# Optimization experiments

Measured on AMD Instinct MI355X. Metric: run time of the kernel, lower is better.

## Reference

```python
import jax, jax.numpy as jnp
import numpy as np

N = 10000
E = 160000
IN_DIM = 128
OUT_DIM = 32
HEADS = 32
H1 = OUT_DIM * 2   # 64 per-head channels in layer 1
H2 = OUT_DIM       # 32 per-head channels in layer 2
NEG_SLOPE = 0.2
EPS = 1e-16  # PyG softmax denominator epsilon


def gat_layer(x, src, dst, W, a_src, a_dst, b, n_nodes, heads, ch):
    # x: [N, F_in], W: [F_in, heads*ch], a_src/a_dst: [heads, ch], b: [ch]
    xp = (x @ W).reshape(n_nodes, heads, ch)                 # [N,H,C]
    alpha_s = jnp.einsum('nhc,hc->nh', xp, a_src)            # [N,H]
    alpha_d = jnp.einsum('nhc,hc->nh', xp, a_dst)            # [N,H]
    e = jax.nn.leaky_relu(alpha_s[src] + alpha_d[dst], NEG_SLOPE)  # [E,H]
    # segment softmax over edges grouped by destination node
    m = jax.ops.segment_max(e, dst, num_segments=n_nodes)    # [N,H]
    e = jnp.exp(e - m[dst])                                  # [E,H]
    s = jax.ops.segment_sum(e, dst, num_segments=n_nodes)    # [N,H]
    alpha = e / (s[dst] + EPS)                               # [E,H]
    msg = alpha[:, :, None] * xp[src]                        # [E,H,C]
    out = jax.ops.segment_sum(msg, dst, num_segments=n_nodes)  # [N,H,C]
    return out.mean(axis=1) + b                              # concat=False: head mean, [N,C]


def setup_inputs() -> dict:
    key = jax.random.key(0)
    ks = jax.random.split(key, 9)
    x = jax.random.normal(ks[0], (N, IN_DIM), dtype=jnp.float32)
    edge_index = jax.random.randint(ks[1], (2, E), 0, N, dtype=jnp.int64)
    W1 = jax.random.normal(ks[2], (IN_DIM, HEADS * H1), dtype=jnp.float32) * 0.1
    a_src1 = jax.random.normal(ks[3], (HEADS, H1), dtype=jnp.float32) * 0.1
    a_dst1 = jax.random.normal(ks[4], (HEADS, H1), dtype=jnp.float32) * 0.1
    b1 = jnp.zeros((H1,), dtype=jnp.float32)
    W2 = jax.random.normal(ks[5], (H1, HEADS * H2), dtype=jnp.float32) * 0.1
    a_src2 = jax.random.normal(ks[6], (HEADS, H2), dtype=jnp.float32) * 0.1
    a_dst2 = jax.random.normal(ks[7], (HEADS, H2), dtype=jnp.float32) * 0.1
    b2 = jnp.zeros((H2,), dtype=jnp.float32)
    return {"x": x, "edge_index": edge_index,
            "W1": W1, "a_src1": a_src1, "a_dst1": a_dst1, "b1": b1,
            "W2": W2, "a_src2": a_src2, "a_dst2": a_dst2, "b2": b2}


def reference(x, edge_index, W1, a_src1, a_dst1, b1, W2, a_src2, a_dst2, b2):
    # flow='source_to_target': messages go edge_index[0] -> edge_index[1]
    src = edge_index[0]
    dst = edge_index[1]
    z1 = jax.nn.elu(gat_layer(x, src, dst, W1, a_src1, a_dst1, b1, N, HEADS, H1))
    z2 = jax.nn.elu(gat_layer(z1, src, dst, W2, a_src2, a_dst2, b2, N, HEADS, H2))
    return jnp.concatenate((z1, z2), axis=-1)  # [N, 96]
```

## Files before the change

### kernel.cpp

```cpp
#include <hip/hip_runtime.h>
#include <hip/hip_bf16.h>

#define NN 10000
#define NE 160000
#define NH 32
#define LRELU_SLOPE 0.2f
#define SM_EPS 1e-16f
#define SM_SHIFT 16.0f

typedef __hip_bfloat16 bf16;
typedef __attribute__((ext_vector_type(8))) __bf16 bf16x8;
typedef __attribute__((ext_vector_type(4))) float f32x4;

__device__ __forceinline__ float bits2f(unsigned int u16) {
    union { unsigned int u; float f; } v; v.u = u16 << 16; return v.f;
}
__device__ __forceinline__ void loadbf8(const bf16* __restrict__ p, float f[8]) {
    uint4 v = *reinterpret_cast<const uint4*>(p);
    f[0] = bits2f(v.x & 0xffffu); f[1] = bits2f(v.x >> 16);
    f[2] = bits2f(v.y & 0xffffu); f[3] = bits2f(v.y >> 16);
    f[4] = bits2f(v.z & 0xffffu); f[5] = bits2f(v.z >> 16);
    f[6] = bits2f(v.w & 0xffffu); f[7] = bits2f(v.w >> 16);
}

__global__ void k_edge_detect(const unsigned int* __restrict__ raw, int* __restrict__ flag) {
    if (threadIdx.x == 0 && blockIdx.x == 0) {
        int z = 1;
        for (int i = 1; i < 32; i += 2) z &= (raw[i] == 0u);
        *flag = z;
    }
}
__global__ void k_edge_norm(const int* __restrict__ raw, const int* __restrict__ flag,
                            int* __restrict__ srcv, int* __restrict__ dstv, int* __restrict__ deg) {
    int e = blockIdx.x * blockDim.x + threadIdx.x;
    if (e < NN) deg[e] = 0;
    if (e >= NE) return;
    if (*flag) { srcv[e] = raw[2 * e]; dstv[e] = raw[2 * (NE + e)]; }
    else       { srcv[e] = raw[e];     dstv[e] = raw[NE + e]; }
}

__global__ void k_hist(const int* __restrict__ dstv, int* __restrict__ deg) {
    int e = blockIdx.x * blockDim.x + threadIdx.x;
    if (e < NE) atomicAdd(&deg[dstv[e]], 1);
}
__global__ void k_scan(const int* __restrict__ deg, int* __restrict__ offs, int* __restrict__ cursor) {
    __shared__ int wsum[16], wpre[16];
    __shared__ int base;
    const int tid = threadIdx.x, lane = tid & 63, wid = tid >> 6;
    if (tid == 0) base = 0;
    __syncthreads();
    for (int chunk = 0; chunk < NN; chunk += 1024) {
        int idx = chunk + tid;
        int v = (idx < NN) ? deg[idx] : 0;
        int s = v;
        #pragma unroll
        for (int off = 1; off < 64; off <<= 1) {
            int t = __shfl_up(s, off);
            if (lane >= off) s += t;
        }
        if (lane == 63) wsum[wid] = s;
        __syncthreads();
        if (wid == 0) {
            int ws = (lane < 16) ? wsum[lane] : 0;
            #pragma unroll
            for (int off = 1; off < 16; off <<= 1) {
                int t = __shfl_up(ws, off);
                if (lane >= off) ws += t;
            }
            if (lane < 16) wpre[lane] = ws;
        }
        __syncthreads();
        int wbase = (wid == 0) ? 0 : wpre[wid - 1];
        int excl = base + wbase + s - v;
        if (idx < NN) { offs[idx] = excl; cursor[idx] = excl; }
        int total = wpre[15];
        __syncthreads();
        if (tid == 0) base += total;
        __syncthreads();
    }
    if (tid == 0) offs[NN] = base;
}
__global__ void k_scatter(const int* __restrict__ srcv, const int* __restrict__ dstv,
                          int* __restrict__ cursor, int* __restrict__ srcs) {
    int e = blockIdx.x * blockDim.x + threadIdx.x;
    if (e < NE) {
        int p = atomicAdd(&cursor[dstv[e]], 1);
        srcs[p] = srcv[e];
    }
}

__global__ void k_prep(const float* __restrict__ X, bf16* __restrict__ Xb,
                       const float* __restrict__ W1, bf16* __restrict__ Wt1,
                       const float* __restrict__ W2, bf16* __restrict__ Wt2) {
    int i = blockIdx.x * blockDim.x + threadIdx.x;
    if (i < NN * 128) { Xb[i] = __float2bfloat16(X[i]); return; }
    i -= NN * 128;
    if (i < 128 * 2048) {
        int k = i / 2048, m = i - k * 2048;
        Wt1[(size_t)m * 128 + k] = __float2bfloat16(W1[i]);
        return;
    }
    i -= 128 * 2048;
    if (i < 64 * 1024) {
        int k = i / 1024, m = i - k * 1024;
        Wt2[(size_t)m * 64 + k] = __float2bfloat16(W2[i]);
    }
}

template<int K, int M, int C>
__global__ __launch_bounds__(256) void k_gemm_mfma(
        const bf16* __restrict__ Xb, const bf16* __restrict__ Wt,
        const float* __restrict__ Asrc, const float* __restrict__ Adst,
        bf16* __restrict__ XPB, float* __restrict__ aS, float* __restrict__ aD) {
    constexpr int BM = 64, BN = 128;
    constexpr int KB = K * 2;
    constexpr int NHB = BN / C;
    constexpr int WPH = C / 32;
    __shared__ char lds[(BM + BN) * KB];
    __shared__ float sredS[4][BM], sredD[4][BM];
    char* lA = lds;
    char* lB = lds + BM * KB;

    const int tid = threadIdx.x;
    const int wv = tid >> 6, ln = tid & 63;
    const int lrow = ln & 15, lkb = ln >> 4;
    const int brow = blockIdx.x * BM;
    const int bcol = blockIdx.y * BN;

    #pragma unroll
    for (int c = 0; c < BM * K / 8 / 256; c++) {
        int it = c * 256 + tid;
        int r = it / (K / 8), kc = (it % (K / 8)) * 8;
        int node = brow + r;
        uint4 v = make_uint4(0u, 0u, 0u, 0u);
        if (node < NN) v = *reinterpret_cast<const uint4*>(&Xb[(size_t)node * K + kc]);
        *reinterpret_cast<uint4*>(lA + ((r * KB + kc * 2) ^ ((r & 7) << 4))) = v;
    }
    #pragma unroll
    for (int c = 0; c < BN * K / 8 / 256; c++) {
        int it = c * 256 + tid;
        int r = it / (K / 8), kc = (it % (K / 8)) * 8;
        uint4 v = *reinterpret_cast<const uint4*>(&Wt[(size_t)(bcol + r) * K + kc]);
        *reinterpret_cast<uint4*>(lB + ((r * KB + kc * 2) ^ ((r & 7) << 4))) = v;
    }
    __syncthreads();

    f32x4 acc[4][2];
    #pragma unroll
    for (int mi = 0; mi < 4; mi++)
        #pragma unroll
        for (int nj = 0; nj < 2; nj++) acc[mi][nj] = (f32x4){0.f, 0.f, 0.f, 0.f};

    #pragma unroll
    for (int ks = 0; ks < K / 32; ks++) {
        const int k0 = ks * 32 + lkb * 8;
        bf16x8 af[4], bfr[2];
        #pragma unroll
        for (int mi = 0; mi < 4; mi++) {
            int r = mi * 16 + lrow;
            af[mi] = *reinterpret_cast<const bf16x8*>(lA + ((r * KB + k0 * 2) ^ ((r & 7) << 4)));
        }
        #pragma unroll
        for (int nj = 0; nj < 2; nj++) {
            int r = wv * 32 + nj * 16 + lrow;
            bfr[nj] = *reinterpret_cast<const bf16x8*>(lB + ((r * KB + k0 * 2) ^ ((r & 7) << 4)));
        }
        #pragma unroll
        for (int mi = 0; mi < 4; mi++)
            #pragma unroll
            for (int nj = 0; nj < 2; nj++)
                acc[mi][nj] = __builtin_amdgcn_mfma_f32_16x16x32_bf16(af[mi], bfr[nj], acc[mi][nj], 0, 0, 0);
    }

    float ar0 = Asrc[bcol + wv * 32 + lrow];
    float ar1 = Asrc[bcol + wv * 32 + 16 + lrow];
    float ad0 = Adst[bcol + wv * 32 + lrow];
    float ad1 = Adst[bcol + wv * 32 + 16 + lrow];

    #pragma unroll
    for (int mi = 0; mi < 4; mi++) {
        #pragma unroll
        for (int r = 0; r < 4; r++) {
            int rowl = mi * 16 + lkb * 4 + r;
            int row = brow + rowl;
            if (row < NN) {
                XPB[(size_t)row * M + bcol + wv * 32 + lrow]      = __float2bfloat16(acc[mi][0][r]);
                XPB[(size_t)row * M + bcol + wv * 32 + 16 + lrow] = __float2bfloat16(acc[mi][1][r]);
            }
            float vs = acc[mi][0][r] * ar0 + acc[mi][1][r] * ar1;
            float vd = acc[mi][0][r] * ad0 + acc[mi][1][r] * ad1;
            vs += __shfl_xor(vs, 1); vd += __shfl_xor(vd, 1);
            vs += __shfl_xor(vs, 2); vd += __shfl_xor(vd, 2);
            vs += __shfl_xor(vs, 4); vd += __shfl_xor(vd, 4);
            vs += __shfl_xor(vs, 8); vd += __shfl_xor(vd, 8);
            if (lrow == 0) {
                sredS[wv][rowl] = vs;
                sredD[wv][rowl] = vd;
            }
        }
    }
    __syncthreads();
    if (tid < BM) {
        int node = brow + tid;
        if (node < NN) {
            #pragma unroll
            for (int hb = 0; hb < NHB; hb++) {
                float ss = 0.f, dd = 0.f;
                #pragma unroll
                for (int w = 0; w < WPH; w++) {
                    ss += sredS[hb * WPH + w][tid];
                    dd += sredD[hb * WPH + w][tid];
                }
                int h = bcol / C + hb;
                aS[node * NH + h] = ss;
                aD[node * NH + h] = dd;
            }
        }
    }
}

template<int C>
__global__ __launch_bounds__(256) void k_agg_slice(
        const bf16* __restrict__ XPB, const float* __restrict__ aS,
        const float* __restrict__ aD, const int* __restrict__ offs,
        const int* __restrict__ srcs, float* __restrict__ P, int sg0) {
    constexpr int M = NH * C;
    constexpr int HPS = 128 / C;
    constexpr int CGH = C / 8;
    const int sg = sg0 + (blockIdx.x & 7);
    const int wid = threadIdx.x >> 6, lane = threadIdx.x & 63;
    const int node = (blockIdx.x >> 3) * 4 + wid;
    const int cg = lane & 15, el = lane >> 4;
    const int hl = cg / CGH;
    const int h = sg * HPS + hl;
    const int col = sg * 128 + cg * 8;
    const int beg = offs[node], end = offs[node + 1];
    const float ad = aD[node * NH + h];
    float acc[8];
    #pragma unroll
    for (int j = 0; j < 8; j++) acc[j] = 0.f;
    float ssum = 0.f;
    for (int i = beg + el; i < end; i += 4) {
        int s = srcs[i];
        float sc = aS[s * NH + h] + ad;
        sc = (sc >= 0.f) ? sc : LRELU_SLOPE * sc;
        float p = __expf(sc - SM_SHIFT);
        ssum += p;
        float xv[8];
        loadbf8(&XPB[(size_t)s * M + col], xv);
        #pragma unroll
        for (int j = 0; j < 8; j++) acc[j] = fmaf(p, xv[j], acc[j]);
    }
    #pragma unroll
    for (int j = 0; j < 8; j++) {
        acc[j] += __shfl_xor(acc[j], 16);
        acc[j] += __shfl_xor(acc[j], 32);
    }
    ssum += __shfl_xor(ssum, 16);
    ssum += __shfl_xor(ssum, 32);
    float r = 1.f / (ssum + SM_EPS);
    #pragma unroll
    for (int j = 0; j < 8; j++) acc[j] *= r;
    #pragma unroll
    for (int j = 0; j < 8; j++) acc[j] += __shfl_xor(acc[j], 8);
    if constexpr (HPS == 4) {
        #pragma unroll
        for (int j = 0; j < 8; j++) acc[j] += __shfl_xor(acc[j], 4);
    }
    if (el == 0 && cg < CGH) {
        float* dst = &P[((size_t)sg * NN + node) * C + cg * 8];
        *reinterpret_cast<float4*>(dst)     = make_float4(acc[0], acc[1], acc[2], acc[3]);
        *reinterpret_cast<float4*>(dst + 4) = make_float4(acc[4], acc[5], acc[6], acc[7]);
    }
}

template<int C, int NS, bool WZ>
__global__ void k_reduce(const float* __restrict__ P, const float* __restrict__ bias,
                         float* __restrict__ out, int col0, bf16* __restrict__ z1b) {
    const int tid = threadIdx.x;
    const int node = blockIdx.x * (256 / C) + tid / C;
    const int c = tid % C;
    float s = 0.f;
    #pragma unroll
    for (int sg = 0; sg < NS; sg++) s += P[((size_t)sg * NN + node) * C + c];
    s = s * (1.0f / NH) + bias[c];
    s = (s > 0.f) ? s : expm1f(s);
    out[(size_t)node * 96 + col0 + c] = s;
    if constexpr (WZ) z1b[(size_t)node * C + c] = __float2bfloat16(s);
}

extern "C" void kernel_launch(void* const* d_in, const int* in_sizes, int n_in,
                              void* d_out, int out_size, void* d_ws, size_t ws_size,
                              hipStream_t stream) {
    const float* x   = (const float*)d_in[0];
    const int*   ei  = (const int*)d_in[1];
    const float* W1  = (const float*)d_in[2];
    const float* as1 = (const float*)d_in[3];
    const float* ad1 = (const float*)d_in[4];
    const float* b1  = (const float*)d_in[5];
    const float* W2  = (const float*)d_in[6];
    const float* as2 = (const float*)d_in[7];
    const float* ad2 = (const float*)d_in[8];
    const float* b2  = (const float*)d_in[9];
    float* out = (float*)d_out;

    char* w = (char*)d_ws;
    size_t off = 0;
    auto alloc = [&](size_t bytes) -> void* {
        void* p = w + off;
        off = (off + bytes + 255) & ~(size_t)255;
        return p;
    };
    bf16*  xpb    = (bf16*)alloc((size_t)NN * 2048 * 2);
    float* aS     = (float*)alloc((size_t)NN * NH * 4);
    float* aD     = (float*)alloc((size_t)NN * NH * 4);
    float* P1     = (float*)alloc((size_t)16 * NN * 64 * 4);
    float* P2     = (float*)alloc((size_t)8 * NN * 32 * 4);
    int*   deg    = (int*)alloc((size_t)NN * 4);
    int*   cursor = (int*)alloc((size_t)NN * 4);
    int*   offs   = (int*)alloc((size_t)(NN + 1) * 4);
    int*   srcs   = (int*)alloc((size_t)NE * 4);
    int*   srcv   = (int*)alloc((size_t)NE * 4);
    int*   dstv   = (int*)alloc((size_t)NE * 4);
    bf16*  Xb     = (bf16*)alloc((size_t)NN * 128 * 2);
    bf16*  Wt1    = (bf16*)alloc((size_t)2048 * 128 * 2);
    bf16*  Wt2    = (bf16*)alloc((size_t)1024 * 64 * 2);
    bf16*  z1b    = (bf16*)alloc((size_t)NN * 64 * 2);
    int*   eflag  = (int*)alloc(256);
    (void)ws_size; (void)in_sizes; (void)n_in; (void)out_size;

    k_edge_detect<<<1, 64, 0, stream>>>((const unsigned int*)ei, eflag);
    k_edge_norm<<<(NE + 255) / 256, 256, 0, stream>>>(ei, eflag, srcv, dstv, deg);
    k_hist<<<NE / 256, 256, 0, stream>>>(dstv, deg);
    k_scan<<<1, 1024, 0, stream>>>(deg, offs, cursor);
    k_scatter<<<NE / 256, 256, 0, stream>>>(srcv, dstv, cursor, srcs);

    k_prep<<<(NN * 128 + 128 * 2048 + 64 * 1024 + 255) / 256, 256, 0, stream>>>(
        x, Xb, W1, Wt1, W2, Wt2);

    k_gemm_mfma<128, 2048, 64><<<dim3((NN + 63) / 64, 2048 / 128), 256, 0, stream>>>(
        Xb, Wt1, as1, ad1, xpb, aS, aD);
    k_agg_slice<64><<<(NN / 4) * 8, 256, 0, stream>>>(xpb, aS, aD, offs, srcs, P1, 0);
    k_agg_slice<64><<<(NN / 4) * 8, 256, 0, stream>>>(xpb, aS, aD, offs, srcs, P1, 8);
    k_reduce<64, 16, true><<<NN / 4, 256, 0, stream>>>(P1, b1, out, 0, z1b);

    k_gemm_mfma<64, 1024, 32><<<dim3((NN + 63) / 64, 1024 / 128), 256, 0, stream>>>(
        z1b, Wt2, as2, ad2, xpb, aS, aD);
    k_agg_slice<32><<<(NN / 4) * 8, 256, 0, stream>>>(xpb, aS, aD, offs, srcs, P2, 0);
    k_reduce<32, 8, false><<<NN / 8, 256, 0, stream>>>(P2, b2, out, 64, nullptr);
}
```

Measured before the change: 252.6 us.

## Precompute edge softmax scores once per layer and prefetch in aggregation

Adds a k_score kernel that computes the exponentiated attention score for every edge and head, plus the per-node reciprocal sum, once per layer. The aggregation slices then read these scores instead of recomputing leaky-relu and exp in each of the 8 or 16 slice launches, and software-prefetch the next source index and score. It also fuses the degree histogram into the edge normalisation kernel, vectorises the reduce kernel to float4, and aliases P2 onto P1. The cost is an extra 20 MB pE buffer that has to be written and read back, in exchange for removing repeated exp work and repeated gathers of aS.

```diff
diff --git a/kernel.cpp b/kernel.cpp
--- a/kernel.cpp
+++ b/kernel.cpp
@@ -12,36 +12,29 @@
 typedef __attribute__((ext_vector_type(8))) __bf16 bf16x8;
 typedef __attribute__((ext_vector_type(4))) float f32x4;
 
-__device__ __forceinline__ float bits2f(unsigned int u16) {
-    union { unsigned int u; float f; } v; v.u = u16 << 16; return v.f;
-}
-__device__ __forceinline__ void loadbf8(const bf16* __restrict__ p, float f[8]) {
-    uint4 v = *reinterpret_cast<const uint4*>(p);
-    f[0] = bits2f(v.x & 0xffffu); f[1] = bits2f(v.x >> 16);
-    f[2] = bits2f(v.y & 0xffffu); f[3] = bits2f(v.y >> 16);
-    f[4] = bits2f(v.z & 0xffffu); f[5] = bits2f(v.z >> 16);
-    f[6] = bits2f(v.w & 0xffffu); f[7] = bits2f(v.w >> 16);
-}
-
-__global__ void k_edge_detect(const unsigned int* __restrict__ raw, int* __restrict__ flag) {
-    if (threadIdx.x == 0 && blockIdx.x == 0) {
+__device__ __forceinline__ float asf(unsigned int u) {
+    union { unsigned int u; float f; } v; v.u = u; return v.f;
+}
+
+__global__ void k_detect_zero(const unsigned int* __restrict__ raw, int* __restrict__ flag,
+                              int* __restrict__ deg) {
+    int i = blockIdx.x * blockDim.x + threadIdx.x;
+    if (i < NN) deg[i] = 0;
+    if (i == 0) {
         int z = 1;
-        for (int i = 1; i < 32; i += 2) z &= (raw[i] == 0u);
+        for (int j = 1; j < 32; j += 2) z &= (raw[j] == 0u);
         *flag = z;
     }
 }
-__global__ void k_edge_norm(const int* __restrict__ raw, const int* __restrict__ flag,
+__global__ void k_norm_hist(const int* __restrict__ raw, const int* __restrict__ flag,
                             int* __restrict__ srcv, int* __restrict__ dstv, int* __restrict__ deg) {
     int e = blockIdx.x * blockDim.x + threadIdx.x;
-    if (e < NN) deg[e] = 0;
     if (e >= NE) return;
-    if (*flag) { srcv[e] = raw[2 * e]; dstv[e] = raw[2 * (NE + e)]; }
-    else       { srcv[e] = raw[e];     dstv[e] = raw[NE + e]; }
-}
-
-__global__ void k_hist(const int* __restrict__ dstv, int* __restrict__ deg) {
-    int e = blockIdx.x * blockDim.x + threadIdx.x;
-    if (e < NE) atomicAdd(&deg[dstv[e]], 1);
+    int s, d;
+    if (*flag) { s = raw[2 * e]; d = raw[2 * (NE + e)]; }
+    else       { s = raw[e];     d = raw[NE + e]; }
+    srcv[e] = s; dstv[e] = d;
+    atomicAdd(&deg[d], 1);
 }
 __global__ void k_scan(const int* __restrict__ deg, int* __restrict__ offs, int* __restrict__ cursor) {
     __shared__ int wsum[16], wpre[16];
@@ -219,10 +212,32 @@
     }
 }
 
+__global__ __launch_bounds__(256) void k_score(
+        const float* __restrict__ aS, const float* __restrict__ aD,
+        const int* __restrict__ offs, const int* __restrict__ srcs,
+        float* __restrict__ pE, float* __restrict__ rinv) {
+    const int wid = threadIdx.x >> 6, lane = threadIdx.x & 63;
+    const int node = blockIdx.x * 4 + wid;
+    const int h = lane & 31, el = lane >> 5;
+    const int beg = offs[node], end = offs[node + 1];
+    const float ad = aD[node * NH + h];
+    float ssum = 0.f;
+    for (int i = beg + el; i < end; i += 2) {
+        int s = srcs[i];
+        float sc = aS[s * NH + h] + ad;
+        sc = (sc >= 0.f) ? sc : LRELU_SLOPE * sc;
+        float p = __expf(sc - SM_SHIFT);
+        pE[i * NH + h] = p;
+        ssum += p;
+    }
+    ssum += __shfl_xor(ssum, 32);
+    if (el == 0) rinv[node * NH + h] = 1.f / (ssum + SM_EPS);
+}
+
 template<int C>
 __global__ __launch_bounds__(256) void k_agg_slice(
-        const bf16* __restrict__ XPB, const float* __restrict__ aS,
-        const float* __restrict__ aD, const int* __restrict__ offs,
+        const bf16* __restrict__ XPB, const float* __restrict__ pE,
+        const float* __restrict__ rinv, const int* __restrict__ offs,
         const int* __restrict__ srcs, float* __restrict__ P, int sg0) {
     constexpr int M = NH * C;
     constexpr int HPS = 128 / C;
@@ -235,30 +250,33 @@
     const int h = sg * HPS + hl;
     const int col = sg * 128 + cg * 8;
     const int beg = offs[node], end = offs[node + 1];
-    const float ad = aD[node * NH + h];
     float acc[8];
     #pragma unroll
     for (int j = 0; j < 8; j++) acc[j] = 0.f;
-    float ssum = 0.f;
-    for (int i = beg + el; i < end; i += 4) {
-        int s = srcs[i];
-        float sc = aS[s * NH + h] + ad;
-        sc = (sc >= 0.f) ? sc : LRELU_SLOPE * sc;
-        float p = __expf(sc - SM_SHIFT);
-        ssum += p;
-        float xv[8];
-        loadbf8(&XPB[(size_t)s * M + col], xv);
-        #pragma unroll
-        for (int j = 0; j < 8; j++) acc[j] = fmaf(p, xv[j], acc[j]);
+    int i = beg + el;
+    int sN = 0; float pN = 0.f;
+    if (i < end) { sN = srcs[i]; pN = pE[i * NH + h]; }
+    while (i < end) {
+        const int s = sN; const float p = pN;
+        const int i2 = i + 4;
+        if (i2 < end) { sN = srcs[i2]; pN = pE[i2 * NH + h]; }
+        uint4 v = *reinterpret_cast<const uint4*>(&XPB[s * M + col]);
+        acc[0] = fmaf(p, asf(v.x << 16),          acc[0]);
+        acc[1] = fmaf(p, asf(v.x & 0xffff0000u),  acc[1]);
+        acc[2] = fmaf(p, asf(v.y << 16),          acc[2]);
+        acc[3] = fmaf(p, asf(v.y & 0xffff0000u),  acc[3]);
+        acc[4] = fmaf(p, asf(v.z << 16),          acc[4]);
+        acc[5] = fmaf(p, asf(v.z & 0xffff0000u),  acc[5]);
+        acc[6] = fmaf(p, asf(v.w << 16),          acc[6]);
+        acc[7] = fmaf(p, asf(v.w & 0xffff0000u),  acc[7]);
+        i = i2;
     }
     #pragma unroll
     for (int j = 0; j < 8; j++) {
         acc[j] += __shfl_xor(acc[j], 16);
         acc[j] += __shfl_xor(acc[j], 32);
     }
-    ssum += __shfl_xor(ssum, 16);
-    ssum += __shfl_xor(ssum, 32);
-    float r = 1.f / (ssum + SM_EPS);
+    const float r = rinv[node * NH + h];
     #pragma unroll
     for (int j = 0; j < 8; j++) acc[j] *= r;
     #pragma unroll
@@ -277,16 +295,33 @@
 template<int C, int NS, bool WZ>
 __global__ void k_reduce(const float* __restrict__ P, const float* __restrict__ bias,
                          float* __restrict__ out, int col0, bf16* __restrict__ z1b) {
+    constexpr int TPN = C / 4;
     const int tid = threadIdx.x;
-    const int node = blockIdx.x * (256 / C) + tid / C;
-    const int c = tid % C;
-    float s = 0.f;
-    #pragma unroll
-    for (int sg = 0; sg < NS; sg++) s += P[((size_t)sg * NN + node) * C + c];
-    s = s * (1.0f / NH) + bias[c];
-    s = (s > 0.f) ? s : expm1f(s);
-    out[(size_t)node * 96 + col0 + c] = s;
-    if constexpr (WZ) z1b[(size_t)node * C + c] = __float2bfloat16(s);
+    const int node = blockIdx.x * (256 / TPN) + tid / TPN;
+    const int c = (tid % TPN) * 4;
+    if (node >= NN) return;
+    float4 s = make_float4(0.f, 0.f, 0.f, 0.f);
+    #pragma unroll
+    for (int sg = 0; sg < NS; sg++) {
+        float4 v = *reinterpret_cast<const float4*>(&P[((size_t)sg * NN + node) * C + c]);
+        s.x += v.x; s.y += v.y; s.z += v.z; s.w += v.w;
+    }
+    float4 b = *reinterpret_cast<const float4*>(&bias[c]);
+    s.x = s.x * (1.0f / NH) + b.x;
+    s.y = s.y * (1.0f / NH) + b.y;
+    s.z = s.z * (1.0f / NH) + b.z;
+    s.w = s.w * (1.0f / NH) + b.w;
+    s.x = (s.x > 0.f) ? s.x : expm1f(s.x);
+    s.y = (s.y > 0.f) ? s.y : expm1f(s.y);
+    s.z = (s.z > 0.f) ? s.z : expm1f(s.z);
+    s.w = (s.w > 0.f) ? s.w : expm1f(s.w);
+    *reinterpret_cast<float4*>(&out[(size_t)node * 96 + col0 + c]) = s;
+    if constexpr (WZ) {
+        bf16 hx[4] = {__float2bfloat16(s.x), __float2bfloat16(s.y),
+                      __float2bfloat16(s.z), __float2bfloat16(s.w)};
+        *reinterpret_cast<uint2*>(&z1b[(size_t)node * C + c]) =
+            *reinterpret_cast<const uint2*>(hx);
+    }
 }
 
 extern "C" void kernel_launch(void* const* d_in, const int* in_sizes, int n_in,
@@ -314,8 +349,10 @@
     bf16*  xpb    = (bf16*)alloc((size_t)NN * 2048 * 2);
     float* aS     = (float*)alloc((size_t)NN * NH * 4);
     float* aD     = (float*)alloc((size_t)NN * NH * 4);
+    float* pE     = (float*)alloc((size_t)NE * NH * 4);
+    float* rinv   = (float*)alloc((size_t)NN * NH * 4);
     float* P1     = (float*)alloc((size_t)16 * NN * 64 * 4);
-    float* P2     = (float*)alloc((size_t)8 * NN * 32 * 4);
+    float* P2     = P1;
     int*   deg    = (int*)alloc((size_t)NN * 4);
     int*   cursor = (int*)alloc((size_t)NN * 4);
     int*   offs   = (int*)alloc((size_t)(NN + 1) * 4);
@@ -329,9 +366,8 @@
     int*   eflag  = (int*)alloc(256);
     (void)ws_size; (void)in_sizes; (void)n_in; (void)out_size;
 
-    k_edge_detect<<<1, 64, 0, stream>>>((const unsigned int*)ei, eflag);
-    k_edge_norm<<<(NE + 255) / 256, 256, 0, stream>>>(ei, eflag, srcv, dstv, deg);
-    k_hist<<<NE / 256, 256, 0, stream>>>(dstv, deg);
+    k_detect_zero<<<(NN + 255) / 256, 256, 0, stream>>>((const unsigned int*)ei, eflag, deg);
+    k_norm_hist<<<NE / 256, 256, 0, stream>>>(ei, eflag, srcv, dstv, deg);
     k_scan<<<1, 1024, 0, stream>>>(deg, offs, cursor);
     k_scatter<<<NE / 256, 256, 0, stream>>>(srcv, dstv, cursor, srcs);
 
@@ -340,12 +376,14 @@
 
     k_gemm_mfma<128, 2048, 64><<<dim3((NN + 63) / 64, 2048 / 128), 256, 0, stream>>>(
         Xb, Wt1, as1, ad1, xpb, aS, aD);
-    k_agg_slice<64><<<(NN / 4) * 8, 256, 0, stream>>>(xpb, aS, aD, offs, srcs, P1, 0);
-    k_agg_slice<64><<<(NN / 4) * 8, 256, 0, stream>>>(xpb, aS, aD, offs, srcs, P1, 8);
-    k_reduce<64, 16, true><<<NN / 4, 256, 0, stream>>>(P1, b1, out, 0, z1b);
+    k_score<<<NN / 4, 256, 0, stream>>>(aS, aD, offs, srcs, pE, rinv);
+    k_agg_slice<64><<<(NN / 4) * 8, 256, 0, stream>>>(xpb, pE, rinv, offs, srcs, P1, 0);
+    k_agg_slice<64><<<(NN / 4) * 8, 256, 0, stream>>>(xpb, pE, rinv, offs, srcs, P1, 8);
+    k_reduce<64, 16, true><<<NN / 16, 256, 0, stream>>>(P1, b1, out, 0, z1b);
 
     k_gemm_mfma<64, 1024, 32><<<dim3((NN + 63) / 64, 1024 / 128), 256, 0, stream>>>(
         z1b, Wt2, as2, ad2, xpb, aS, aD);
-    k_agg_slice<32><<<(NN / 4) * 8, 256, 0, stream>>>(xpb, aS, aD, offs, srcs, P2, 0);
-    k_reduce<32, 8, false><<<NN / 8, 256, 0, stream>>>(P2, b2, out, 64, nullptr);
-}
+    k_score<<<NN / 4, 256, 0, stream>>>(aS, aD, offs, srcs, pE, rinv);
+    k_agg_slice<32><<<(NN / 4) * 8, 256, 0, stream>>>(xpb, pE, rinv, offs, srcs, P2, 0);
+    k_reduce<32, 8, false><<<(NN * 8 + 255) / 256, 256, 0, stream>>>(P2, b2, out, 64, nullptr);
+}
```

Result: slower. 276.0 us (+9.3%).
